# Kernel optimization log

Measured on AMD Instinct MI355X. Metric: run time of the kernel, lower is better.

The kernel has to match this reference:

```python
import jax, jax.numpy as jnp
import numpy as np

M0 = 0.05
R = 2
SIZE = (64, 64)
LIMS = ((1.0, 64.0), (1.0, 64.0))


def _make_grid():
    # torch make_grid: linspace reversed on H axis, forward on W axis,
    # cartesian_prod(ys, xs) then column-swap -> points are (x, y)
    H, W = SIZE
    ys = jnp.linspace(LIMS[0][1], LIMS[0][0], H)
    xs = jnp.linspace(LIMS[1][0], LIMS[1][1], W)
    yy, xx = jnp.meshgrid(ys, xs, indexing="ij")
    return jnp.stack([xx.ravel(), yy.ravel()], axis=-1)  # [HW, 2]


def _pairwise_dist(grid):
    # [HW, HW] euclidean distance (r == 2 path of cal_dist)
    d2 = jnp.sum((grid[:, None, :] - grid[None, :, :]) ** 2, axis=-1)
    return jnp.sqrt(d2)


def setup_inputs() -> dict:
    key = jax.random.key(0)
    x = jax.random.uniform(key, (4, 3, 64, 64), dtype=jnp.float32)
    return {"x": x}


def reference(x):
    B, C, H, W = x.shape
    HW = H * W
    weight = x.reshape(B, C, HW)                      # [B, C, HW]
    bound = M0 * jnp.sum(weight, -1, keepdims=True)   # [B, C, 1]

    # data-dependent max_k (torch does this eagerly via .item(); keep eager)
    sw_cumsum = jnp.cumsum(jnp.sort(weight, -1), -1)  # [B, C, HW]
    max_k = int(jnp.max(jnp.sum(sw_cumsum < bound, -1))) + 1
    max_k = min(max_k, HW)

    # KNN over the fixed grid distance matrix
    dist = _pairwise_dist(_make_grid())               # [HW, HW]
    neg_d, knn_index = jax.lax.top_k(-dist, max_k)    # smallest-k, ascending
    knn_dist = -neg_d                                 # [HW, max_k]

    # weighted DTM using KNN (r == 2)
    knn_weight = weight[:, :, knn_index]              # [B, C, HW, max_k]
    cum_w = jnp.cumsum(knn_weight, -1)                # [B, C, HW, max_k]
    bound4 = bound[..., None]                         # [B, C, 1, 1]
    # searchsorted(left): first idx with cum_w >= bound == count of cum_w < bound
    k = jnp.sum(cum_w < bound4, -1, keepdims=True)    # [B, C, HW, 1]
    k = jnp.clip(k, 0, max_k - 1)
    r_dist = (knn_dist ** 2)[None, None]              # [1, 1, HW, max_k]
    cum_dist = jnp.cumsum(r_dist * knn_weight, -1)
    val = jnp.take_along_axis(cum_dist + r_dist * (bound4 - cum_w), k, axis=-1)
    dtm = jnp.sqrt(val[..., 0] / bound)               # [B, C, HW]
    return dtm.reshape(B, C, H, W)
```

## Files before the change

kernel.cpp:

```cpp
#include <hip/hip_runtime.h>
#include <stdint.h>


#define HW     4096
#define NOFF   16129
#define NPAD   16384
#define NBIN   8192
#define NCHUNK 16

struct Ent { uint32_t off; float d2; };
struct Tables { Ent e[NPAD]; };

constexpr Tables make_tables() {
    Tables t{};
    int cnt[NBIN] = {};
    for (int idx = 0; idx < NOFF; ++idx) {
        int di = idx / 127 - 63, dj = idx % 127 - 63;
        cnt[di * di + dj * dj]++;
    }
    int run = 0;
    for (int b = 0; b < NBIN; ++b) { int c = cnt[b]; cnt[b] = run; run += c; }
    for (int idx = 0; idx < NOFF; ++idx) {
        int di = idx / 127 - 63, dj = idx % 127 - 63;
        int d2 = di * di + dj * dj;
        int pos = cnt[d2]++;
        t.e[pos].off = (uint32_t)((di + 63) << 7) | (uint32_t)(dj + 63);
        t.e[pos].d2  = (float)d2;
    }
    for (int p = NOFF; p < NPAD; ++p) {
        t.e[p].off = 0u;
        t.e[p].d2  = 0.0f;
    }
    return t;
}

__device__ const Tables g_t = make_tables();

__global__ __launch_bounds__(1024, 8) void dtm_kernel(const float* __restrict__ x,
                                                      float* __restrict__ out) {
    __shared__ float  w[HW + 64];
    __shared__ float2 summ[NCHUNK][64];
    __shared__ float  red[NCHUNK];

    int bc   = blockIdx.x >> 6;
    int pi   = blockIdx.x & 63;
    int tid  = threadIdx.x;
    int lane = tid & 63;
    int wv   = tid >> 6;

    const float4* xb = (const float4*)(x + (size_t)bc * HW);
    float4 v = xb[tid];
    const uint2* gt = (const uint2*)g_t.e;
    uint2 ev = gt[(wv << 6) | lane];

    ((float4*)w)[tid] = v;
    if (wv == 0) w[HW + lane] = 0.f;
    float s = (v.x + v.y) + (v.z + v.w);
    #pragma unroll
    for (int off = 32; off >= 1; off >>= 1) s += __shfl_down(s, off, 64);
    if (lane == 0) red[wv] = s;
    __syncthreads();

    float mass = 0.f, d2m = 0.f;
    #pragma unroll 8
    for (int k = 0; k < 64; ++k) {
        uint32_t eo = (uint32_t)__builtin_amdgcn_readlane((int)ev.x, k);
        float d2 = __uint_as_float((uint32_t)__builtin_amdgcn_readlane((int)ev.y, k));
        int row = pi + (int)(eo >> 7) - 63;
        unsigned rbase = (((unsigned)row < 64u) ? (unsigned)row : 64u) << 6;
        int qj = lane + (int)(eo & 127u) - 63;
        float wq = w[rbase + ((unsigned)qj & 63u)];
        wq = ((unsigned)qj < 64u) ? wq : 0.f;
        mass += wq;
        d2m = fmaf(d2, wq, d2m);
    }
    summ[wv][lane] = make_float2(mass, d2m);
    __syncthreads();
    if (wv != 0) return;

    float bound = 0.f;
    #pragma unroll
    for (int i = 0; i < NCHUNK; ++i) bound += red[i];
    bound *= 0.05f;

    float rem = bound, cumd = 0.f;
    int cstar = NCHUNK - 1;
    bool found = false;
    #pragma unroll
    for (int c = 0; c < NCHUNK - 1; ++c) {
        float2 p = summ[c][lane];
        bool cross = (!found) && (p.x >= rem);
        cstar = cross ? c : cstar;
        bool adv = (!found) && (!cross);
        rem  = adv ? rem - p.x : rem;
        cumd = adv ? cumd + p.y : cumd;
        found = found || cross;
    }

    float val = 0.f;
    bool done = false;
    int pos = cstar << 6;
    #pragma unroll 8
    for (int k = 0; k < 64; ++k) {
        uint2 e = gt[pos + k];
        int qi = pi + (int)((e.x >> 7) & 127u) - 63;
        int qj = lane + (int)(e.x & 127u) - 63;
        bool ok = ((unsigned)qi < 64u) && ((unsigned)qj < 64u) && !done;
        float wq = w[(((unsigned)qi & 63u) << 6) | ((unsigned)qj & 63u)];
        wq = ok ? wq : 0.f;
        float d2 = __uint_as_float(e.y);
        bool cross = (!done) && (wq >= rem);
        val  = cross ? fmaf(d2, rem, cumd) : val;
        done = done || cross;
        cumd = fmaf(d2, wq, cumd);
        rem -= wq;
    }
    pos += 64;

    while (__any(!done)) {
        int idx = pos < NPAD ? pos : NPAD - 1;
        uint2 e = gt[idx];
        int qi = pi + (int)((e.x >> 7) & 127u) - 63;
        int qj = lane + (int)(e.x & 127u) - 63;
        bool ok = ((unsigned)qi < 64u) && ((unsigned)qj < 64u) && !done;
        float wq = w[(((unsigned)qi & 63u) << 6) | ((unsigned)qj & 63u)];
        wq = ok ? wq : 0.f;
        float d2 = __uint_as_float(e.y);
        bool cross = (!done) && ((wq >= rem) || (pos >= NPAD));
        val  = cross ? fmaf(d2, rem, cumd) : val;
        done = done || cross;
        cumd = fmaf(d2, wq, cumd);
        rem -= wq;
        pos++;
    }

    out[(size_t)bc * HW + (pi << 6) + lane] = sqrtf(val / bound);
}

extern "C" void kernel_launch(void* const* d_in, const int* in_sizes, int n_in,
                              void* d_out, int out_size, void* d_ws, size_t ws_size,
                              hipStream_t stream) {
    const float* x = (const float*)d_in[0];
    float* out = (float*)d_out;
    int BC = in_sizes[0] / HW;
    dtm_kernel<<<BC * 64, 1024, 0, stream>>>(x, out);
}
```

Measured before the change: 75.93 us.

## Exploit offset symmetry with windowed row-pair tables and fewer threads per block

Replaces the full 127x127 sorted offset table with a quadrant table of (|di|,|dj|) groups. Each group sums the four symmetric neighbours, using a precomputed per-block row-pair buffer of x[pi-d]+x[pi+d] restricted to a distance window. Only the window is chunk-summarised, and the fallback walk reads global memory directly. Block size is halved to 512 threads, each loading two float4s. This cuts shared-memory gathers and table entries per pixel, at the cost of extra setup work and the assumption that the crossing usually falls inside the window.

```diff
diff --git a/kernel.cpp b/kernel.cpp
--- a/kernel.cpp
+++ b/kernel.cpp
@@ -3,44 +3,66 @@
 
 
 #define HW     4096
-#define NOFF   16129
-#define NPAD   16384
 #define NBIN   8192
+#define WIN_D2 360
+#define DMAX   18
+#define HSTR   100
+#define HOFF   18
+#define WROWS  19
+#define WPN    (WROWS * HSTR)
 #define NCHUNK 16
+#define NG     4096
 
-struct Ent { uint32_t off; float d2; };
-struct Tables { Ent e[NPAD]; };
+struct GM { uint32_t de; float d2; };
 
-constexpr Tables make_tables() {
-    Tables t{};
+constexpr int cnt_win_groups() {
+    int n = 0;
+    for (int d = 0; d < 64; ++d)
+        for (int e = 0; e < 64; ++e)
+            if (d * d + e * e <= WIN_D2) ++n;
+    return n;
+}
+constexpr int cnt_win_entries() {
+    int n = 0;
+    for (int d = -63; d < 64; ++d)
+        for (int e = -63; e < 64; ++e)
+            if (d * d + e * e <= WIN_D2) ++n;
+    return n;
+}
+constexpr int NWIN  = cnt_win_groups();
+constexpr int GPC   = (NWIN + NCHUNK - 1) / NCHUNK;
+constexpr int NWINP = GPC * NCHUNK;
+static_assert(cnt_win_entries() >= 1024, "window must cover worst crossing");
+static_assert(NWIN <= NWINP && NWINP - NWIN < GPC, "pad only in last chunk");
+
+struct GTabs { GM g[NG]; GM w[NWINP]; };
+
+constexpr GTabs make_tabs() {
+    GTabs t{};
     int cnt[NBIN] = {};
-    for (int idx = 0; idx < NOFF; ++idx) {
-        int di = idx / 127 - 63, dj = idx % 127 - 63;
-        cnt[di * di + dj * dj]++;
-    }
+    for (int d = 0; d < 64; ++d)
+        for (int e = 0; e < 64; ++e) cnt[d * d + e * e]++;
     int run = 0;
     for (int b = 0; b < NBIN; ++b) { int c = cnt[b]; cnt[b] = run; run += c; }
-    for (int idx = 0; idx < NOFF; ++idx) {
-        int di = idx / 127 - 63, dj = idx % 127 - 63;
-        int d2 = di * di + dj * dj;
-        int pos = cnt[d2]++;
-        t.e[pos].off = (uint32_t)((di + 63) << 7) | (uint32_t)(dj + 63);
-        t.e[pos].d2  = (float)d2;
-    }
-    for (int p = NOFF; p < NPAD; ++p) {
-        t.e[p].off = 0u;
-        t.e[p].d2  = 0.0f;
-    }
+    for (int d = 0; d < 64; ++d)
+        for (int e = 0; e < 64; ++e) {
+            int d2 = d * d + e * e;
+            int pos = cnt[d2]++;
+            unsigned code = (e == 0) ? 1u : 0u;
+            t.g[pos].de = (uint32_t)d | ((uint32_t)e << 6) | (code << 12);
+            t.g[pos].d2 = (float)d2;
+        }
+    for (int i = 0; i < NWIN; ++i) t.w[i] = t.g[i];
+    for (int i = NWIN; i < NWINP; ++i) { t.w[i].de = (2u << 12); t.w[i].d2 = (float)WIN_D2; }
     return t;
 }
+__device__ const GTabs g_t = make_tabs();
 
-__device__ const Tables g_t = make_tables();
-
-__global__ __launch_bounds__(1024, 8) void dtm_kernel(const float* __restrict__ x,
-                                                      float* __restrict__ out) {
-    __shared__ float  w[HW + 64];
+__global__ __launch_bounds__(512, 8) void dtm_kernel(const float* __restrict__ x,
+                                                     float* __restrict__ out) {
+    __shared__ float  wpair[WPN];
     __shared__ float2 summ[NCHUNK][64];
-    __shared__ float  red[NCHUNK];
+    __shared__ float  red[8];
 
     int bc   = blockIdx.x >> 6;
     int pi   = blockIdx.x & 63;
@@ -48,39 +70,61 @@
     int lane = tid & 63;
     int wv   = tid >> 6;
 
-    const float4* xb = (const float4*)(x + (size_t)bc * HW);
-    float4 v = xb[tid];
-    const uint2* gt = (const uint2*)g_t.e;
-    uint2 ev = gt[(wv << 6) | lane];
+    const float* __restrict__ xs = x + (size_t)bc * HW;
 
-    ((float4*)w)[tid] = v;
-    if (wv == 0) w[HW + lane] = 0.f;
-    float s = (v.x + v.y) + (v.z + v.w);
+    const float4* xb = (const float4*)xs;
+    float4 a0 = xb[tid];
+    float4 a1 = xb[tid + 512];
+    float s = ((a0.x + a0.y) + (a0.z + a0.w)) + ((a1.x + a1.y) + (a1.z + a1.w));
     #pragma unroll
     for (int off = 32; off >= 1; off >>= 1) s += __shfl_down(s, off, 64);
     if (lane == 0) red[wv] = s;
+
+    for (int idx = tid; idx < WPN; idx += 512) {
+        int d = idx / HSTR;
+        int c = idx - d * HSTR;
+        int j = c - HOFF;
+        float v = 0.f;
+        if ((unsigned)j < 64u) {
+            int rm = pi - d, rp = pi + d;
+            if (rm >= 0) v += xs[rm * 64 + j];
+            if (d > 0 && rp < 64) v += xs[rp * 64 + j];
+        }
+        wpair[idx] = v;
+    }
+
+    const GM* __restrict__ mw = g_t.w;
+    int li = lane < GPC ? lane : GPC - 1;
+    GM mv0 = mw[(2 * wv)     * GPC + li];
+    GM mv1 = mw[(2 * wv + 1) * GPC + li];
     __syncthreads();
 
-    float mass = 0.f, d2m = 0.f;
-    #pragma unroll 8
-    for (int k = 0; k < 64; ++k) {
-        uint32_t eo = (uint32_t)__builtin_amdgcn_readlane((int)ev.x, k);
-        float d2 = __uint_as_float((uint32_t)__builtin_amdgcn_readlane((int)ev.y, k));
-        int row = pi + (int)(eo >> 7) - 63;
-        unsigned rbase = (((unsigned)row < 64u) ? (unsigned)row : 64u) << 6;
-        int qj = lane + (int)(eo & 127u) - 63;
-        float wq = w[rbase + ((unsigned)qj & 63u)];
-        wq = ((unsigned)qj < 64u) ? wq : 0.f;
-        mass += wq;
-        d2m = fmaf(d2, wq, d2m);
+    #pragma unroll
+    for (int h = 0; h < 2; ++h) {
+        GM mv = h ? mv1 : mv0;
+        float m0 = 0.f, dm0 = 0.f;
+        #pragma unroll 5
+        for (int k = 0; k < GPC; ++k) {
+            uint32_t de = (uint32_t)__builtin_amdgcn_readlane((int)mv.de, k);
+            float d2 = __uint_as_float((uint32_t)__builtin_amdgcn_readlane(__float_as_int(mv.d2), k));
+            int d = de & 63, e = (de >> 6) & 63;
+            unsigned code = de >> 12;
+            float sc = code == 0 ? 1.f : (code == 1 ? 0.5f : 0.f);
+            int base = d * HSTR + HOFF;
+            float g1 = wpair[base + lane - e];
+            float g2 = wpair[base + lane + e];
+            float m = sc * (g1 + g2);
+            m0 += m;
+            dm0 = fmaf(d2, m, dm0);
+        }
+        summ[2 * wv + h][lane] = make_float2(m0, dm0);
     }
-    summ[wv][lane] = make_float2(mass, d2m);
     __syncthreads();
     if (wv != 0) return;
 
     float bound = 0.f;
     #pragma unroll
-    for (int i = 0; i < NCHUNK; ++i) bound += red[i];
+    for (int i = 0; i < 8; ++i) bound += red[i];
     bound *= 0.05f;
 
     float rem = bound, cumd = 0.f;
@@ -92,44 +136,51 @@
         bool cross = (!found) && (p.x >= rem);
         cstar = cross ? c : cstar;
         bool adv = (!found) && (!cross);
-        rem  = adv ? rem - p.x : rem;
-        cumd = adv ? cumd + p.y : cumd;
+        rem   = adv ? rem - p.x : rem;
+        cumd  = adv ? cumd + p.y : cumd;
         found = found || cross;
     }
 
     float val = 0.f;
     bool done = false;
-    int pos = cstar << 6;
-    #pragma unroll 8
-    for (int k = 0; k < 64; ++k) {
-        uint2 e = gt[pos + k];
-        int qi = pi + (int)((e.x >> 7) & 127u) - 63;
-        int qj = lane + (int)(e.x & 127u) - 63;
-        bool ok = ((unsigned)qi < 64u) && ((unsigned)qj < 64u) && !done;
-        float wq = w[(((unsigned)qi & 63u) << 6) | ((unsigned)qj & 63u)];
-        wq = ok ? wq : 0.f;
-        float d2 = __uint_as_float(e.y);
+    int g0 = cstar * GPC;
+    #pragma unroll 4
+    for (int k = 0; k < GPC; ++k) {
+        GM mm = mw[g0 + k];
+        int d = mm.de & 63, e = (mm.de >> 6) & 63;
+        unsigned code = mm.de >> 12;
+        float sc = code == 0 ? 1.f : (code == 1 ? 0.5f : 0.f);
+        int base = d * HSTR + HOFF + lane;
+        float m = sc * (wpair[base - e] + wpair[base + e]);
+        float wq = done ? 0.f : m;
         bool cross = (!done) && (wq >= rem);
-        val  = cross ? fmaf(d2, rem, cumd) : val;
+        val  = cross ? fmaf(mm.d2, rem, cumd) : val;
         done = done || cross;
-        cumd = fmaf(d2, wq, cumd);
+        cumd = fmaf(mm.d2, wq, cumd);
         rem -= wq;
     }
-    pos += 64;
 
+    int pos = g0 + GPC; if (pos > NWIN) pos = NWIN;
+    const GM* __restrict__ mg = g_t.g;
     while (__any(!done)) {
-        int idx = pos < NPAD ? pos : NPAD - 1;
-        uint2 e = gt[idx];
-        int qi = pi + (int)((e.x >> 7) & 127u) - 63;
-        int qj = lane + (int)(e.x & 127u) - 63;
-        bool ok = ((unsigned)qi < 64u) && ((unsigned)qj < 64u) && !done;
-        float wq = w[(((unsigned)qi & 63u) << 6) | ((unsigned)qj & 63u)];
-        wq = ok ? wq : 0.f;
-        float d2 = __uint_as_float(e.y);
-        bool cross = (!done) && ((wq >= rem) || (pos >= NPAD));
-        val  = cross ? fmaf(d2, rem, cumd) : val;
+        int ix = pos < NG ? pos : NG - 1;
+        GM mm = mg[ix];
+        int d = mm.de & 63, e = (mm.de >> 6) & 63;
+        float sc = ((mm.de >> 12) == 1u) ? 0.5f : 1.f;
+        if (d == 0) sc *= 0.5f;
+        int rm = pi - d, rp = pi + d;
+        int cm = lane - e, cp = lane + e;
+        float m = 0.f;
+        if (rm >= 0 && cm >= 0) m += xs[rm * 64 + cm];
+        if (rm >= 0 && cp < 64) m += xs[rm * 64 + cp];
+        if (rp < 64 && cm >= 0) m += xs[rp * 64 + cm];
+        if (rp < 64 && cp < 64) m += xs[rp * 64 + cp];
+        m *= sc;
+        float wq = done ? 0.f : m;
+        bool cross = (!done) && ((wq >= rem) || (pos >= NG));
+        val  = cross ? fmaf(mm.d2, rem, cumd) : val;
         done = done || cross;
-        cumd = fmaf(d2, wq, cumd);
+        cumd = fmaf(mm.d2, wq, cumd);
         rem -= wq;
         pos++;
     }
@@ -143,5 +194,5 @@
     const float* x = (const float*)d_in[0];
     float* out = (float*)d_out;
     int BC = in_sizes[0] / HW;
-    dtm_kernel<<<BC * 64, 1024, 0, stream>>>(x, out);
+    dtm_kernel<<<BC * 64, 512, 0, stream>>>(x, out);
 }
```

Result: faster. 62.32 us (-17.9%).
